# Performance work log

Measured on AMD Instinct MI355X. Metric: run time of the kernel, lower is better.

## Reference

```python
import jax, jax.numpy as jnp
import numpy as np

D = 2048
H = 16
DH = D // H  # 128
THETA = 10000.0

def _rope(x, pos):
    # x: (..., S, DH); pos: (S,) absolute positions
    freqs = 1.0 / THETA ** (jnp.arange(0, DH, 2, dtype=jnp.float32) / DH)  # (DH/2,)
    emb = pos[:, None].astype(jnp.float32) * freqs[None, :]                # (S, DH/2)
    cos = jnp.concatenate([jnp.cos(emb), jnp.cos(emb)], axis=-1)          # tile like torch .repeat(...,2)
    sin = jnp.concatenate([jnp.sin(emb), jnp.sin(emb)], axis=-1)
    x1, x2 = x[..., : DH // 2], x[..., DH // 2 :]
    rot = jnp.concatenate([-x2, x1], axis=-1)  # rotate_half
    return x * cos + rot * sin

def setup_inputs() -> dict:
    key = jax.random.key(0)
    ks = jax.random.split(key, 4)
    B, S = 2, 2048
    return {
        "x": jax.random.normal(ks[0], (B, S, D), jnp.float32),
        "wq": 0.01 * jax.random.normal(ks[1], (D, D), jnp.float32),
        "wkv": 0.01 * jax.random.normal(ks[2], (D, 2 * DH), jnp.float32),
        "wo": 0.01 * jax.random.normal(ks[3], (D, D), jnp.float32),
        "past_length": 0,
    }

def reference(x, wq, wkv, wo, past_length):
    B, S, _ = x.shape
    Q = x @ wq.T                       # (B,S,D)
    KV = x @ wkv                       # (B,S,2*DH)
    K, V = KV[..., :DH], KV[..., DH:]  # single shared KV head (B,S,DH)
    # no kv_cache (prefill): S_full = past_length + S with past_length=0
    S_full = past_length + S
    q = Q.reshape(B, S, H, DH).transpose(0, 2, 1, 3)   # (B,H,S,DH)
    q = _rope(q, past_length + jnp.arange(S))
    k = _rope(K, jnp.arange(S_full))                    # (B,S_full,DH), unreplicated
    scores = jnp.einsum('bhsd,btd->bhst', q, k) / np.float32(np.sqrt(DH))
    i = jnp.arange(S)[:, None]
    j = jnp.arange(S_full)[None, :]
    causal = j <= i + past_length                       # tril(diagonal=past_length)
    scores = jnp.where(causal[None, None], scores, -jnp.inf)
    attn = jax.nn.softmax(scores, axis=-1)
    o = jnp.einsum('bhst,btd->bhsd', attn, V)           # (B,H,S,DH)
    o = o.transpose(0, 2, 1, 3).reshape(B, S, D)
    out = o @ wo.T
    return (out, K, V)  # output + updated kv cache
```

## Files before the change

kernel.cpp:

```cpp
#include <hip/hip_runtime.h>
#include <hip/hip_bf16.h>
#include <cstdint>


typedef __attribute__((ext_vector_type(8))) __bf16 bf16x8;
typedef __attribute__((ext_vector_type(4))) float f32x4;
typedef __attribute__((ext_vector_type(16))) float f32x16;
typedef __attribute__((ext_vector_type(4))) float floatv4;
typedef __attribute__((ext_vector_type(4))) unsigned short ushortv4;
typedef __attribute__((ext_vector_type(4))) unsigned int uintv4;

__device__ __forceinline__ unsigned short f2bf(float f) {
    union { float f; unsigned u; } v; v.f = f;
    unsigned r = v.u + 0x7fffu + ((v.u >> 16) & 1u);
    return (unsigned short)(r >> 16);
}

__device__ __forceinline__ unsigned pk2(float a, float b) {
    return (unsigned)f2bf(a) | ((unsigned)f2bf(b) << 16);
}

__device__ __forceinline__ f32x16 zero16() {
    f32x16 z;
#pragma unroll
    for (int i = 0; i < 16; ++i) z[i] = 0.f;
    return z;
}

#define GLL16(g, l)                                                                   \
    __builtin_amdgcn_global_load_lds(                                                 \
        (const __attribute__((address_space(1))) void*)(uintptr_t)(g),                \
        (__attribute__((address_space(3))) void*)(unsigned)(uintptr_t)(l), 16, 0, 0)

__global__ __launch_bounds__(256) void cast_bf16_k(const float* __restrict__ src,
                                                   unsigned short* __restrict__ dst, int n4) {
    int i = blockIdx.x * 256 + threadIdx.x;
    if (i >= n4) return;
    floatv4 v = reinterpret_cast<const floatv4*>(src)[i];
    ushortv4 o;
    o.x = f2bf(v.x); o.y = f2bf(v.y); o.z = f2bf(v.z); o.w = f2bf(v.w);
    reinterpret_cast<ushortv4*>(dst)[i] = o;
}

__global__ __launch_bounds__(256) void cast_t_wkv_k(const float* __restrict__ src,
                                                    unsigned short* __restrict__ dst) {
    int i = blockIdx.x * 256 + threadIdx.x;
    int k = i >> 8, j = i & 255;
    dst[j * 2048 + k] = f2bf(src[i]);
}

__global__ __launch_bounds__(256) void gemm_bt(const unsigned short* __restrict__ A,
                                               const unsigned short* __restrict__ B,
                                               float* __restrict__ C,
                                               int M, int N, int K) {
    __shared__ __align__(16) unsigned short As[4096];
    __shared__ __align__(16) unsigned short Bs[4096];
    const int tid  = threadIdx.x;
    const int lane = tid & 63;
    const int wid  = tid >> 6;
    const int wr   = wid >> 1;
    const int wc   = wid & 1;
    const size_t row0 = (size_t)blockIdx.y * 128;
    const size_t col0 = (size_t)blockIdx.x * 128;
    f32x4 acc[4][4];
#pragma unroll
    for (int m = 0; m < 4; ++m)
#pragma unroll
        for (int n = 0; n < 4; ++n) acc[m][n] = (f32x4){0.f, 0.f, 0.f, 0.f};

    const int srow = tid >> 2;
    const int scol = (tid & 3) << 3;
    const unsigned short* Ag = A + (row0 + srow) * (size_t)K + scol;
    const unsigned short* Bg = B + (col0 + srow) * (size_t)K + scol;
    unsigned short* AsW = &As[wid << 9];
    unsigned short* BsW = &Bs[wid << 9];

    const int lrow = lane & 15;
    const int lk   = (lane >> 4) << 3;

    for (int k0 = 0; k0 < K; k0 += 32) {
        GLL16(Ag + k0, AsW);
        GLL16(Ag + k0 + (size_t)64 * K, AsW + 2048);
        GLL16(Bg + k0, BsW);
        GLL16(Bg + k0 + (size_t)64 * K, BsW + 2048);
        __syncthreads();
        bf16x8 af[4], bfr[4];
#pragma unroll
        for (int m = 0; m < 4; ++m)
            af[m] = *reinterpret_cast<const bf16x8*>(&As[(wr * 64 + m * 16 + lrow) * 32 + lk]);
#pragma unroll
        for (int n = 0; n < 4; ++n)
            bfr[n] = *reinterpret_cast<const bf16x8*>(&Bs[(wc * 64 + n * 16 + lrow) * 32 + lk]);
#pragma unroll
        for (int m = 0; m < 4; ++m)
#pragma unroll
            for (int n = 0; n < 4; ++n)
                acc[m][n] = __builtin_amdgcn_mfma_f32_16x16x32_bf16(af[m], bfr[n], acc[m][n], 0, 0, 0);
        __syncthreads();
    }
    const size_t orow0 = row0 + wr * 64 + ((lane >> 4) << 2);
    const size_t ocol  = col0 + wc * 64 + lrow;
#pragma unroll
    for (int m = 0; m < 4; ++m)
#pragma unroll
        for (int n = 0; n < 4; ++n)
#pragma unroll
            for (int r = 0; r < 4; ++r)
                C[(orow0 + m * 16 + r) * (size_t)N + ocol + n * 16] = acc[m][n][r];
}

__global__ __launch_bounds__(256) void rope_pack_k(const float* __restrict__ Qf,
                                                   const float* __restrict__ KVf,
                                                   unsigned short* __restrict__ Qb,
                                                   unsigned short* __restrict__ Kb,
                                                   unsigned short* __restrict__ Vt,
                                                   float* __restrict__ Kout,
                                                   float* __restrict__ Vout) {
    const int row = blockIdx.x;
    const int b = row >> 11;
    const int s = row & 2047;
    const int t = threadIdx.x;
    const float* qrow = Qf + (size_t)row * 2048;
#pragma unroll
    for (int it = 0; it < 4; ++it) {
        int p = t + it * 256;
        int h = p >> 6;
        int i = p & 63;
        float fr  = exp2f(-(float)i * 0.20762050593045858f);
        float ang = (float)s * fr;
        float sn, c;
        sincosf(ang, &sn, &c);
        float x1 = qrow[h * 128 + i];
        float x2 = qrow[h * 128 + i + 64];
        size_t qb = (((size_t)(b * 16 + h)) * 2048 + s) * 128;
        Qb[qb + i]      = f2bf(x1 * c - x2 * sn);
        Qb[qb + i + 64] = f2bf(x2 * c + x1 * sn);
    }
    const float* kvrow = KVf + (size_t)row * 256;
    if (t < 128) {
        float kv = kvrow[t];
        float vv = kvrow[128 + t];
        Kout[(size_t)row * 128 + t] = kv;
        Vout[(size_t)row * 128 + t] = vv;
        Vt[((size_t)(b * 128 + t)) * 2048 + s] = f2bf(vv);
    }
    if (t < 64) {
        float fr  = exp2f(-(float)t * 0.20762050593045858f);
        float ang = (float)s * fr;
        float sn, c;
        sincosf(ang, &sn, &c);
        float x1 = kvrow[t];
        float x2 = kvrow[t + 64];
        size_t ko = ((size_t)b * 2048 + s) * 128;
        Kb[ko + t]      = f2bf(x1 * c - x2 * sn);
        Kb[ko + t + 64] = f2bf(x2 * c + x1 * sn);
    }
}

__global__ __launch_bounds__(256, 2) void attn_k(const unsigned short* __restrict__ Qb,
                                                 const unsigned short* __restrict__ Kb,
                                                 const unsigned short* __restrict__ Vt,
                                                 unsigned short* __restrict__ Ob) {
    const int g = 15 - blockIdx.x;
    const int h = blockIdx.y, b = blockIdx.z;
    const int lane = threadIdx.x & 63;
    const int w = threadIdx.x >> 6;
    const int j = 4 * g + w;
    const int q0 = j * 32;
    const int lq = lane & 31;
    const int hl = lane >> 5;
    const int kofs = hl * 8;
    const int my_nkt = 2 * g + 1 + (w >> 1);
    const int NKT = 2 * g + 2;

    __shared__ __align__(16) unsigned short Ks[8192];
    __shared__ __align__(16) unsigned short Vs[8192];

    const unsigned short* kbB = Kb + (size_t)b * 2048 * 128;
    const unsigned short* vtB = Vt + (size_t)b * 128 * 2048;
    const float csc = 0.12751782377892224f;

    int k_r[4], k_gc[4], v_d[4], v_kg[4];
    unsigned short *kdst[4], *vdst[4];
#pragma unroll
    for (int c = 0; c < 4; ++c) {
        int G = w * 256 + c * 64 + lane;
        int r = G >> 4;
        int gc = (G & 15) ^ (r & 15);
        k_r[c] = r; k_gc[c] = gc;
        v_d[c] = r * 2 + (gc >> 3); v_kg[c] = gc & 7;
        kdst[c] = Ks + (w * 2048 + c * 512);
        vdst[c] = Vs + (w * 2048 + c * 512);
    }

    const unsigned short* qp = Qb + (((size_t)(b * 16 + h)) * 2048 + q0 + lq) * 128 + kofs;
    bf16x8 qf[8];
#pragma unroll
    for (int c = 0; c < 8; ++c)
        qf[c] = *reinterpret_cast<const bf16x8*>(qp + 16 * c);

    f32x16 O[4];
#pragma unroll
    for (int dt = 0; dt < 4; ++dt) O[dt] = zero16();
    float m = -1e30f, l = 0.f;

    for (int kt = 0; kt < NKT; ++kt) {
#pragma unroll
        for (int c = 0; c < 4; ++c) {
            GLL16(kbB + (size_t)(64 * kt + k_r[c]) * 128 + k_gc[c] * 8, kdst[c]);
            GLL16(vtB + (size_t)v_d[c] * 2048 + kt * 64 + v_kg[c] * 8, vdst[c]);
        }
        __syncthreads();
        if (kt < my_nkt) {
            bf16x8 kf0[8], kf1[8];
            const int r0 = lq, r1 = lq + 32;
#pragma unroll
            for (int c = 0; c < 8; ++c) {
                kf0[c] = *reinterpret_cast<const bf16x8*>(
                    (const char*)Ks + r0 * 256 + (((2 * c + hl) ^ (r0 & 15)) * 16));
                kf1[c] = *reinterpret_cast<const bf16x8*>(
                    (const char*)Ks + r1 * 256 + (((2 * c + hl) ^ (r1 & 15)) * 16));
            }
            f32x16 S0 = zero16(), S1 = zero16();
#pragma unroll
            for (int c = 0; c < 8; ++c) {
                S0 = __builtin_amdgcn_mfma_f32_32x32x16_bf16(kf0[c], qf[c], S0, 0, 0, 0);
                S1 = __builtin_amdgcn_mfma_f32_32x32x16_bf16(kf1[c], qf[c], S1, 0, 0, 0);
            }
            float sc[32];
            const bool lastt = (kt == my_nkt - 1);
#pragma unroll
            for (int s = 0; s < 2; ++s)
#pragma unroll
                for (int r = 0; r < 16; ++r) {
                    float v = (s ? S1[r] : S0[r]) * csc;
                    if (lastt) {
                        int key = 64 * kt + 32 * s + (r & 3) + 8 * (r >> 2) + 4 * hl;
                        if (key > q0 + lq) v = -3.0e38f;
                    }
                    sc[16 * s + r] = v;
                }
            float tm[16];
#pragma unroll
            for (int i = 0; i < 16; ++i) tm[i] = fmaxf(sc[i], sc[i + 16]);
#pragma unroll
            for (int st = 8; st > 0; st >>= 1)
#pragma unroll
                for (int i = 0; i < st; ++i) tm[i] = fmaxf(tm[i], tm[i + st]);
            float mt = fmaxf(tm[0], __shfl_xor(tm[0], 32));
            float mn = fmaxf(m, mt);
            float corr = __builtin_amdgcn_exp2f(m - mn);
            m = mn;
#pragma unroll
            for (int i = 0; i < 32; ++i) sc[i] = __builtin_amdgcn_exp2f(sc[i] - mn);
            float ts[16];
#pragma unroll
            for (int i = 0; i < 16; ++i) ts[i] = sc[i] + sc[i + 16];
#pragma unroll
            for (int st = 8; st > 0; st >>= 1)
#pragma unroll
                for (int i = 0; i < st; ++i) ts[i] += ts[i + st];
            l = l * corr + ts[0] + __shfl_xor(ts[0], 32);
#pragma unroll
            for (int dt = 0; dt < 4; ++dt)
#pragma unroll
                for (int r = 0; r < 16; ++r) O[dt][r] *= corr;
            unsigned pw[4][4];
#pragma unroll
            for (int s = 0; s < 2; ++s)
#pragma unroll
                for (int c2 = 0; c2 < 2; ++c2) {
                    const int rb = 16 * s + 8 * c2;
                    unsigned X0 = pk2(sc[rb + 0], sc[rb + 1]);
                    unsigned X1 = pk2(sc[rb + 2], sc[rb + 3]);
                    unsigned X2 = pk2(sc[rb + 4], sc[rb + 5]);
                    unsigned X3 = pk2(sc[rb + 6], sc[rb + 7]);
                    unsigned y0 = __shfl_xor(X0, 32);
                    unsigned y1 = __shfl_xor(X1, 32);
                    unsigned y2 = __shfl_xor(X2, 32);
                    unsigned y3 = __shfl_xor(X3, 32);
                    const int kc = 2 * s + c2;
                    pw[kc][0] = hl ? y2 : X0;
                    pw[kc][1] = hl ? y3 : X1;
                    pw[kc][2] = hl ? X2 : y0;
                    pw[kc][3] = hl ? X3 : y1;
                }
            const int vrow_lo = lq >> 1;
            const int vpar8 = (lq & 1) * 8;
#pragma unroll
            for (int kc = 0; kc < 4; ++kc) {
                uintv4 u;
                u.x = pw[kc][0]; u.y = pw[kc][1]; u.z = pw[kc][2]; u.w = pw[kc][3];
                bf16x8 pf = __builtin_bit_cast(bf16x8, u);
                const int gcl = vpar8 + 2 * kc + hl;
#pragma unroll
                for (int dt = 0; dt < 4; ++dt) {
                    const int vrow = 16 * dt + vrow_lo;
                    bf16x8 vf = *reinterpret_cast<const bf16x8*>(
                        (const char*)Vs + vrow * 256 + ((gcl ^ vrow_lo) * 16));
                    O[dt] = __builtin_amdgcn_mfma_f32_32x32x16_bf16(vf, pf, O[dt], 0, 0, 0);
                }
            }
        }
        __syncthreads();
    }

    float invl = 1.f / l;
    unsigned short* ob = Ob + ((size_t)(b * 2048 + q0 + lq)) * 2048 + h * 128;
#pragma unroll
    for (int dt = 0; dt < 4; ++dt)
#pragma unroll
        for (int gg = 0; gg < 4; ++gg) {
            ushortv4 ov;
            ov.x = f2bf(O[dt][4 * gg + 0] * invl);
            ov.y = f2bf(O[dt][4 * gg + 1] * invl);
            ov.z = f2bf(O[dt][4 * gg + 2] * invl);
            ov.w = f2bf(O[dt][4 * gg + 3] * invl);
            *reinterpret_cast<ushortv4*>(ob + 32 * dt + 8 * gg + 4 * hl) = ov;
        }
}

extern "C" void kernel_launch(void* const* d_in, const int* in_sizes, int n_in,
                              void* d_out, int out_size, void* d_ws, size_t ws_size,
                              hipStream_t stream) {
    const float* x   = (const float*)d_in[0];
    const float* wq  = (const float*)d_in[1];
    const float* wkv = (const float*)d_in[2];
    const float* wo  = (const float*)d_in[3];

    float* out  = (float*)d_out;
    float* Kout = out + 8388608;
    float* Vout = Kout + 524288;

    char* ws = (char*)d_ws;
    unsigned short* xb   = (unsigned short*)(ws + 0);
    unsigned short* wqb  = (unsigned short*)(ws + 16777216);
    unsigned short* wkvT = (unsigned short*)(ws + 25165824);
    unsigned short* wob  = (unsigned short*)(ws + 26214400);
    float*          KVf  = (float*)(ws + 34603008);
    float*          Qf   = (float*)(ws + 38797312);
    unsigned short* Qb   = (unsigned short*)(ws + 0);
    unsigned short* Kb   = (unsigned short*)(ws + 16777216);
    unsigned short* Vt   = (unsigned short*)(ws + 17825792);
    unsigned short* Ob   = (unsigned short*)(ws + 34603008);

    cast_bf16_k<<<8192, 256, 0, stream>>>(x,  xb,  2097152);
    cast_bf16_k<<<4096, 256, 0, stream>>>(wq, wqb, 1048576);
    cast_bf16_k<<<4096, 256, 0, stream>>>(wo, wob, 1048576);
    cast_t_wkv_k<<<2048, 256, 0, stream>>>(wkv, wkvT);

    gemm_bt<<<dim3(2, 32),  256, 0, stream>>>(xb, wkvT, KVf, 4096, 256,  2048);
    gemm_bt<<<dim3(16, 32), 256, 0, stream>>>(xb, wqb,  Qf,  4096, 2048, 2048);

    rope_pack_k<<<4096, 256, 0, stream>>>(Qf, KVf, Qb, Kb, Vt, Kout, Vout);

    attn_k<<<dim3(16, 16, 2), 256, 0, stream>>>(Qb, Kb, Vt, Ob);

    gemm_bt<<<dim3(16, 32), 256, 0, stream>>>(Ob, wob, out, 4096, 2048, 2048);
}
```

Before: 386.6 us.

## Double-buffer K/V tiles in LDS to prefetch the next tile during compute

The attention kernel now keeps two LDS buffers each for K and V. It issues the direct-to-LDS loads for tile kt+1 before computing on tile kt, with a prologue that loads the first tile. The goal is to hide global-memory latency behind the QK and PV MFMA work and to drop one barrier per iteration. In exchange, LDS use per block doubles to 64KB, which could limit the two-blocks-per-CU occupancy requested by the launch bounds.

```diff
diff --git a/kernel.cpp b/kernel.cpp
--- a/kernel.cpp
+++ b/kernel.cpp
@@ -173,15 +173,14 @@
     const int my_nkt = 2 * g + 1 + (w >> 1);
     const int NKT = 2 * g + 2;
 
-    __shared__ __align__(16) unsigned short Ks[8192];
-    __shared__ __align__(16) unsigned short Vs[8192];
+    __shared__ __align__(16) unsigned short Ks[2][8192];
+    __shared__ __align__(16) unsigned short Vs[2][8192];
 
     const unsigned short* kbB = Kb + (size_t)b * 2048 * 128;
     const unsigned short* vtB = Vt + (size_t)b * 128 * 2048;
     const float csc = 0.12751782377892224f;
 
     int k_r[4], k_gc[4], v_d[4], v_kg[4];
-    unsigned short *kdst[4], *vdst[4];
 #pragma unroll
     for (int c = 0; c < 4; ++c) {
         int G = w * 256 + c * 64 + lane;
@@ -189,9 +188,8 @@
         int gc = (G & 15) ^ (r & 15);
         k_r[c] = r; k_gc[c] = gc;
         v_d[c] = r * 2 + (gc >> 3); v_kg[c] = gc & 7;
-        kdst[c] = Ks + (w * 2048 + c * 512);
-        vdst[c] = Vs + (w * 2048 + c * 512);
-    }
+    }
+    const int dstoff = w * 2048;
 
     const unsigned short* qp = Qb + (((size_t)(b * 16 + h)) * 2048 + q0 + lq) * 128 + kofs;
     bf16x8 qf[8];
@@ -204,22 +202,34 @@
     for (int dt = 0; dt < 4; ++dt) O[dt] = zero16();
     float m = -1e30f, l = 0.f;
 
+#pragma unroll
+    for (int c = 0; c < 4; ++c) {
+        GLL16(kbB + (size_t)k_r[c] * 128 + k_gc[c] * 8, &Ks[0][dstoff + c * 512]);
+        GLL16(vtB + (size_t)v_d[c] * 2048 + v_kg[c] * 8, &Vs[0][dstoff + c * 512]);
+    }
+    __syncthreads();
+
+    int cur = 0;
     for (int kt = 0; kt < NKT; ++kt) {
-#pragma unroll
-        for (int c = 0; c < 4; ++c) {
-            GLL16(kbB + (size_t)(64 * kt + k_r[c]) * 128 + k_gc[c] * 8, kdst[c]);
-            GLL16(vtB + (size_t)v_d[c] * 2048 + kt * 64 + v_kg[c] * 8, vdst[c]);
+        if (kt + 1 < NKT) {
+            const int nxt = cur ^ 1;
+#pragma unroll
+            for (int c = 0; c < 4; ++c) {
+                GLL16(kbB + (size_t)(64 * (kt + 1) + k_r[c]) * 128 + k_gc[c] * 8,
+                      &Ks[nxt][dstoff + c * 512]);
+                GLL16(vtB + (size_t)v_d[c] * 2048 + (kt + 1) * 64 + v_kg[c] * 8,
+                      &Vs[nxt][dstoff + c * 512]);
+            }
         }
-        __syncthreads();
         if (kt < my_nkt) {
             bf16x8 kf0[8], kf1[8];
             const int r0 = lq, r1 = lq + 32;
 #pragma unroll
             for (int c = 0; c < 8; ++c) {
                 kf0[c] = *reinterpret_cast<const bf16x8*>(
-                    (const char*)Ks + r0 * 256 + (((2 * c + hl) ^ (r0 & 15)) * 16));
+                    (const char*)&Ks[cur][0] + r0 * 256 + (((2 * c + hl) ^ (r0 & 15)) * 16));
                 kf1[c] = *reinterpret_cast<const bf16x8*>(
-                    (const char*)Ks + r1 * 256 + (((2 * c + hl) ^ (r1 & 15)) * 16));
+                    (const char*)&Ks[cur][0] + r1 * 256 + (((2 * c + hl) ^ (r1 & 15)) * 16));
             }
             f32x16 S0 = zero16(), S1 = zero16();
 #pragma unroll
@@ -297,12 +307,13 @@
                 for (int dt = 0; dt < 4; ++dt) {
                     const int vrow = 16 * dt + vrow_lo;
                     bf16x8 vf = *reinterpret_cast<const bf16x8*>(
-                        (const char*)Vs + vrow * 256 + ((gcl ^ vrow_lo) * 16));
+                        (const char*)&Vs[cur][0] + vrow * 256 + ((gcl ^ vrow_lo) * 16));
                     O[dt] = __builtin_amdgcn_mfma_f32_32x32x16_bf16(vf, pf, O[dt], 0, 0, 0);
                 }
             }
         }
         __syncthreads();
+        cur ^= 1;
     }
 
     float invl = 1.f / l;
```

After: 384.4 us. About the same (-0.6%).
